# Kernel optimization log

Hardware: AMD Instinct MI355X
Metric: run time of the kernel (lower is better)

The kernel has to match this reference:

```python
import jax, jax.numpy as jnp
import numpy as np

N_NODES = 100000
N_EDGES = 1600000
F_IN = 64
HID = 64
N_ACT = 8


def gcn_conv(x, edge_index, W, b):
    # PyG GCNConv: h = x @ W; add self-loops; norm = deg^{-1/2}[src]*deg^{-1/2}[dst];
    # out[dst] += norm * h[src]; out += b
    n = x.shape[0]
    h = x @ W  # [N, out]
    row = jnp.concatenate([edge_index[0], jnp.arange(n)])  # src (+ self loops)
    col = jnp.concatenate([edge_index[1], jnp.arange(n)])  # dst (+ self loops)
    deg = jax.ops.segment_sum(jnp.ones_like(col, dtype=h.dtype), col, num_segments=n)
    dinv = jnp.where(deg > 0, jax.lax.rsqrt(deg), 0.0)
    norm = dinv[row] * dinv[col]  # [E+N]
    msg = h[row] * norm[:, None]  # gather + scale
    out = jax.ops.segment_sum(msg, col, num_segments=n)  # scatter-add
    return out + b


def setup_inputs() -> dict:
    key = jax.random.key(0)
    ks = jax.random.split(key, 8)
    x = jax.random.normal(ks[0], (N_NODES, F_IN), dtype=jnp.float32)
    edge_index = jax.random.randint(ks[1], (2, N_EDGES), 0, N_NODES, dtype=jnp.int64)
    def glorot(k, fan_in, fan_out):
        s = jnp.sqrt(6.0 / (fan_in + fan_out))
        return jax.random.uniform(k, (fan_in, fan_out), jnp.float32, -s, s)
    W1 = glorot(ks[2], F_IN, HID)
    b1 = jnp.zeros((HID,), jnp.float32)
    W2 = glorot(ks[3], HID, HID)
    b2 = jnp.zeros((HID,), jnp.float32)
    Wfc = glorot(ks[4], HID, N_ACT)
    bfc = jnp.zeros((N_ACT,), jnp.float32)
    return {"x": x, "edge_index": edge_index, "W1": W1, "b1": b1,
            "W2": W2, "b2": b2, "Wfc": Wfc, "bfc": bfc}


def reference(x, edge_index, W1, b1, W2, b2, Wfc, bfc):
    h = jax.nn.relu(gcn_conv(x, edge_index, W1, b1))
    h = jax.nn.relu(gcn_conv(h, edge_index, W2, b2))
    return h @ Wfc + bfc  # Q-values per node: [N, num_actions]
```

## Files before the change

kernel.cpp:

```cpp
#include <hip/hip_runtime.h>
#include <hip/hip_fp16.h>


#define F 64
#define NACT 8
#define BSH 9
#define BNODES 512
#define CAP 10240
#define EPB 2048

__global__ __launch_bounds__(256) void k_init(int* flag, int* cursor) {
  if (threadIdx.x == 0) *flag = 1;
  cursor[threadIdx.x] = 0;
}

__global__ __launch_bounds__(256) void k_detect(const unsigned int* __restrict__ w, int* flag, int E) {
  int i = blockIdx.x * 256 + threadIdx.x;
  if (i < E && w[2 * i + 1] != 0u) *flag = 0;
}

__device__ __forceinline__ int edge_row(const unsigned int* w, int flag, int e, int E) {
  return flag ? (int)w[2 * e] : (int)w[e];
}
__device__ __forceinline__ int edge_col(const unsigned int* w, int flag, int e, int E) {
  return flag ? (int)w[2 * E + 2 * e] : (int)w[E + e];
}

__global__ __launch_bounds__(256) void k_scatterE(const unsigned int* __restrict__ w,
    const int* __restrict__ flag, int* __restrict__ cursor, unsigned int* __restrict__ slab, int E) {
  __shared__ int hist[256];
  __shared__ int base[256];
  const int tid = threadIdx.x;
  const int fl = *flag;
  hist[tid] = 0;
  __syncthreads();
  int pk[8], bb[8], lr[8];
  const int e0 = blockIdx.x * EPB;
#pragma unroll 8
  for (int j = 0; j < 8; ++j) {
    int e = e0 + j * 256 + tid;
    bb[j] = -1;
    if (e < E) {
      int c = edge_col(w, fl, e, E);
      int s = edge_row(w, fl, e, E);
      int b = c >> BSH;
      pk[j] = (unsigned)s | ((unsigned)(c & (BNODES - 1)) << 17);
      bb[j] = b;
      lr[j] = atomicAdd(&hist[b], 1);
    }
  }
  __syncthreads();
  int h = hist[tid];
  if (h > 0) base[tid] = atomicAdd(&cursor[tid], h);
  __syncthreads();
#pragma unroll 8
  for (int j = 0; j < 8; ++j) {
    if (bb[j] >= 0) {
      slab[(size_t)bb[j] * CAP + base[bb[j]] + lr[j]] = (unsigned)pk[j];
    }
  }
}

__global__ __launch_bounds__(64) void k_slabscan(const int* __restrict__ cursor,
    int* __restrict__ bucketBase, int* __restrict__ csr_off, int NB, int n, int E) {
  int t = threadIdx.x;
  int per = (NB + 63) / 64;
  int base = t * per;
  int local = 0;
  for (int i = 0; i < per; ++i) if (base + i < NB) local += cursor[base + i];
  int inc = local;
  for (int off = 1; off < 64; off <<= 1) {
    int vv = __shfl_up(inc, off);
    if (t >= off) inc += vv;
  }
  int run = inc - local;
  for (int i = 0; i < per; ++i) if (base + i < NB) { bucketBase[base + i] = run; run += cursor[base + i]; }
  if (t == 63) { bucketBase[NB] = inc; csr_off[n] = E; }
}

__global__ __launch_bounds__(256) void k_bucketcsr(const unsigned int* __restrict__ slab,
    const int* __restrict__ bucketBase, int* __restrict__ csr_off, float* __restrict__ dinv,
    int* __restrict__ csr_src, int n) {
  __shared__ int cnt[BNODES];
  __shared__ int off[BNODES];
  __shared__ int sA[256], sB[256];
  const int tid = threadIdx.x;
  const int b = blockIdx.x;
  const int csrbeg = bucketBase[b];
  const int cntb = bucketBase[b + 1] - csrbeg;
  const unsigned int* sl = &slab[(size_t)b * CAP];
  cnt[tid] = 0;
  cnt[tid + 256] = 0;
  __syncthreads();
  for (int i = tid; i < cntb; i += 256) {
    atomicAdd(&cnt[sl[i] >> 17], 1);
  }
  __syncthreads();
  int c0 = cnt[2 * tid], c1 = cnt[2 * tid + 1];
  int p = c0 + c1;
  sA[tid] = p;
  __syncthreads();
  int* srcb = sA;
  int* dstb = sB;
  for (int o = 1; o < 256; o <<= 1) {
    int v = srcb[tid];
    if (tid >= o) v += srcb[tid - o];
    __syncthreads();
    dstb[tid] = v;
    __syncthreads();
    int* t2 = srcb; srcb = dstb; dstb = t2;
  }
  int ex2 = srcb[tid] - p;
  off[2 * tid] = ex2;
  off[2 * tid + 1] = ex2 + c0;
  __syncthreads();
  int v0 = (b << BSH) + 2 * tid;
  if (v0 < n) { csr_off[v0] = csrbeg + off[2 * tid]; dinv[v0] = rsqrtf((float)(c0 + 1)); }
  if (v0 + 1 < n) { csr_off[v0 + 1] = csrbeg + off[2 * tid + 1]; dinv[v0 + 1] = rsqrtf((float)(c1 + 1)); }
  __syncthreads();
  for (int i = tid; i < cntb; i += 256) {
    unsigned int pk = sl[i];
    int dl = pk >> 17;
    int pos = atomicAdd(&off[dl], 1);
    csr_src[csrbeg + pos] = (int)(pk & 0x1FFFFu);
  }
}

__device__ __forceinline__ ushort4 packh4(float a, float b, float c, float d) {
  ushort4 r;
  r.x = __half_as_ushort(__float2half_rn(a));
  r.y = __half_as_ushort(__float2half_rn(b));
  r.z = __half_as_ushort(__float2half_rn(c));
  r.w = __half_as_ushort(__float2half_rn(d));
  return r;
}

__device__ __forceinline__ void addrow8(float* a, uint4 g) {
  union { uint4 u; __half2 h[4]; } u;
  u.u = g;
#pragma unroll
  for (int i = 0; i < 4; ++i) {
    float2 f = __half22float2(u.h[i]);
    a[2 * i] += f.x;
    a[2 * i + 1] += f.y;
  }
}

__global__ __launch_bounds__(256) void k_gemm_h(const float* __restrict__ X, const float* __restrict__ W,
    const float* __restrict__ dinv, unsigned short* __restrict__ Gh, int n) {
  __shared__ float xst[F * 68];
  __shared__ float wsh[F * F];
  const int tid = threadIdx.x;
  const int row0 = blockIdx.x * 64;
  for (int i = tid * 4; i < F * F; i += 1024)
    *(float4*)&wsh[i] = *(const float4*)&W[i];
  for (int i = tid * 4; i < 64 * F; i += 1024) {
    int r = i >> 6, k = i & 63;
    float4 v = make_float4(0.f, 0.f, 0.f, 0.f);
    if (row0 + r < n) v = *(const float4*)&X[(size_t)(row0 + r) * F + k];
    xst[(k + 0) * 68 + r] = v.x;
    xst[(k + 1) * 68 + r] = v.y;
    xst[(k + 2) * 68 + r] = v.z;
    xst[(k + 3) * 68 + r] = v.w;
  }
  __syncthreads();
  const int tc = tid & 15;
  const int tr = tid >> 4;
  float a00 = 0.f, a01 = 0.f, a02 = 0.f, a03 = 0.f;
  float a10 = 0.f, a11 = 0.f, a12 = 0.f, a13 = 0.f;
  float a20 = 0.f, a21 = 0.f, a22 = 0.f, a23 = 0.f;
  float a30 = 0.f, a31 = 0.f, a32 = 0.f, a33 = 0.f;
  const float* xp = &xst[tr * 4];
  const float* wp = &wsh[tc * 4];
#pragma unroll 8
  for (int k = 0; k < F; ++k) {
    float4 xv = *(const float4*)&xp[k * 68];
    float4 wv = *(const float4*)&wp[k * F];
    a00 = fmaf(xv.x, wv.x, a00); a01 = fmaf(xv.x, wv.y, a01);
    a02 = fmaf(xv.x, wv.z, a02); a03 = fmaf(xv.x, wv.w, a03);
    a10 = fmaf(xv.y, wv.x, a10); a11 = fmaf(xv.y, wv.y, a11);
    a12 = fmaf(xv.y, wv.z, a12); a13 = fmaf(xv.y, wv.w, a13);
    a20 = fmaf(xv.z, wv.x, a20); a21 = fmaf(xv.z, wv.y, a21);
    a22 = fmaf(xv.z, wv.z, a22); a23 = fmaf(xv.z, wv.w, a23);
    a30 = fmaf(xv.w, wv.x, a30); a31 = fmaf(xv.w, wv.y, a31);
    a32 = fmaf(xv.w, wv.z, a32); a33 = fmaf(xv.w, wv.w, a33);
  }
  const int gc = tc * 4;
  int gr = row0 + tr * 4;
  if (gr + 0 < n) { float d = dinv[gr + 0]; *(ushort4*)&Gh[(size_t)(gr + 0) * F + gc] = packh4(a00 * d, a01 * d, a02 * d, a03 * d); }
  if (gr + 1 < n) { float d = dinv[gr + 1]; *(ushort4*)&Gh[(size_t)(gr + 1) * F + gc] = packh4(a10 * d, a11 * d, a12 * d, a13 * d); }
  if (gr + 2 < n) { float d = dinv[gr + 2]; *(ushort4*)&Gh[(size_t)(gr + 2) * F + gc] = packh4(a20 * d, a21 * d, a22 * d, a23 * d); }
  if (gr + 3 < n) { float d = dinv[gr + 3]; *(ushort4*)&Gh[(size_t)(gr + 3) * F + gc] = packh4(a30 * d, a31 * d, a32 * d, a33 * d); }
}

__global__ __launch_bounds__(256) void k_gather_h(const int* __restrict__ csr_off,
    const int* __restrict__ csr_src, const unsigned short* __restrict__ Gh,
    const float* __restrict__ dinv, const float* __restrict__ b, float* __restrict__ H, int n) {
  int v = blockIdx.x * 32 + (threadIdx.x >> 3);
  if (v >= n) return;
  int l = threadIdx.x & 7;
  const uint4* Gv = (const uint4*)Gh;
  float a[8] = {0.f, 0.f, 0.f, 0.f, 0.f, 0.f, 0.f, 0.f};
  addrow8(a, Gv[(size_t)v * 8 + l]);
  int beg = csr_off[v], end = csr_off[v + 1];
  int j = beg;
  for (; j + 4 <= end; j += 4) {
    int s0 = csr_src[j], s1 = csr_src[j + 1], s2 = csr_src[j + 2], s3 = csr_src[j + 3];
    uint4 g0 = Gv[(size_t)s0 * 8 + l];
    uint4 g1 = Gv[(size_t)s1 * 8 + l];
    uint4 g2 = Gv[(size_t)s2 * 8 + l];
    uint4 g3 = Gv[(size_t)s3 * 8 + l];
    addrow8(a, g0); addrow8(a, g1); addrow8(a, g2); addrow8(a, g3);
  }
  for (; j < end; ++j) addrow8(a, Gv[(size_t)csr_src[j] * 8 + l]);
  float d = dinv[v];
  float4 b0 = *(const float4*)&b[l * 8];
  float4 b1 = *(const float4*)&b[l * 8 + 4];
  float4 o0, o1;
  o0.x = fmaxf(fmaf(a[0], d, b0.x), 0.f);
  o0.y = fmaxf(fmaf(a[1], d, b0.y), 0.f);
  o0.z = fmaxf(fmaf(a[2], d, b0.z), 0.f);
  o0.w = fmaxf(fmaf(a[3], d, b0.w), 0.f);
  o1.x = fmaxf(fmaf(a[4], d, b1.x), 0.f);
  o1.y = fmaxf(fmaf(a[5], d, b1.y), 0.f);
  o1.z = fmaxf(fmaf(a[6], d, b1.z), 0.f);
  o1.w = fmaxf(fmaf(a[7], d, b1.w), 0.f);
  *(float4*)&H[(size_t)v * F + l * 8] = o0;
  *(float4*)&H[(size_t)v * F + l * 8 + 4] = o1;
}

__global__ __launch_bounds__(256) void k_gather_fc(const int* __restrict__ csr_off,
    const int* __restrict__ csr_src, const unsigned short* __restrict__ Gh,
    const float* __restrict__ dinv, const float* __restrict__ bias,
    const float* __restrict__ Wfc, const float* __restrict__ bfc,
    float* __restrict__ OUT, int n) {
  __shared__ float wsh[F * 9];
  __shared__ float bs[NACT];
  const int tid = threadIdx.x;
  for (int i = tid; i < F * NACT; i += 256) wsh[(i >> 3) * 9 + (i & 7)] = Wfc[i];
  if (tid < NACT) bs[tid] = bfc[tid];
  __syncthreads();
  int v = blockIdx.x * 32 + (tid >> 3);
  int l = tid & 7;
  if (v >= n) return;
  const uint4* Gv = (const uint4*)Gh;
  float a[8] = {0.f, 0.f, 0.f, 0.f, 0.f, 0.f, 0.f, 0.f};
  addrow8(a, Gv[(size_t)v * 8 + l]);
  int beg = csr_off[v], end = csr_off[v + 1];
  int j = beg;
  for (; j + 4 <= end; j += 4) {
    int s0 = csr_src[j], s1 = csr_src[j + 1], s2 = csr_src[j + 2], s3 = csr_src[j + 3];
    uint4 g0 = Gv[(size_t)s0 * 8 + l];
    uint4 g1 = Gv[(size_t)s1 * 8 + l];
    uint4 g2 = Gv[(size_t)s2 * 8 + l];
    uint4 g3 = Gv[(size_t)s3 * 8 + l];
    addrow8(a, g0); addrow8(a, g1); addrow8(a, g2); addrow8(a, g3);
  }
  for (; j < end; ++j) addrow8(a, Gv[(size_t)csr_src[j] * 8 + l]);
  float d = dinv[v];
  float q[NACT] = {0.f, 0.f, 0.f, 0.f, 0.f, 0.f, 0.f, 0.f};
#pragma unroll
  for (int jj = 0; jj < 8; ++jj) {
    float h = fmaxf(fmaf(a[jj], d, bias[l * 8 + jj]), 0.f);
    const float* wr = &wsh[(l * 8 + jj) * 9];
#pragma unroll
    for (int aa = 0; aa < NACT; ++aa) q[aa] = fmaf(h, wr[aa], q[aa]);
  }
#pragma unroll
  for (int m = 1; m < 8; m <<= 1) {
#pragma unroll
    for (int aa = 0; aa < NACT; ++aa) q[aa] += __shfl_xor(q[aa], m);
  }
  OUT[(size_t)v * NACT + l] = q[l] + bs[l];
}

extern "C" void kernel_launch(void* const* d_in, const int* in_sizes, int n_in,
                              void* d_out, int out_size, void* d_ws, size_t ws_size,
                              hipStream_t stream) {
  const float* x = (const float*)d_in[0];
  const unsigned int* ew = (const unsigned int*)d_in[1];
  const float* W1 = (const float*)d_in[2];
  const float* b1 = (const float*)d_in[3];
  const float* W2 = (const float*)d_in[4];
  const float* b2 = (const float*)d_in[5];
  const float* Wfc = (const float*)d_in[6];
  const float* bfc = (const float*)d_in[7];
  float* out = (float*)d_out;
  const int n = in_sizes[0] / F;
  const int E = in_sizes[1] / 2;
  const int NB = (n + BNODES - 1) >> BSH;

  char* base = (char*)d_ws;
  size_t off = 0;
  auto alloc = [&](size_t bytes) { void* p = base + off; off += (bytes + 255) & ~(size_t)255; return p; };
  int* flag = (int*)alloc(4);
  int* cursor = (int*)alloc(256 * 4);
  int* bucketBase = (int*)alloc((size_t)(NB + 1) * 4);
  int* csr_off = (int*)alloc((size_t)(n + 1) * 4);
  float* dinv = (float*)alloc((size_t)n * 4);
  unsigned int* slab = (unsigned int*)alloc((size_t)NB * CAP * 4);
  int* csr_src = (int*)alloc((size_t)E * 4);
  unsigned short* Gh = (unsigned short*)alloc((size_t)n * F * 2);
  float* H = (float*)alloc((size_t)n * F * 4);

  const int gbE = (E + 255) / 256;
  const int gbSc = (E + EPB - 1) / EPB;
  const int gbRow = (n + 63) / 64;
  const int gbGa = (n + 31) / 32;

  hipLaunchKernelGGL(k_init, dim3(1), dim3(256), 0, stream, flag, cursor);
  hipLaunchKernelGGL(k_detect, dim3(gbE), dim3(256), 0, stream, ew, flag, E);
  hipLaunchKernelGGL(k_scatterE, dim3(gbSc), dim3(256), 0, stream, ew, flag, cursor, slab, E);
  hipLaunchKernelGGL(k_slabscan, dim3(1), dim3(64), 0, stream, cursor, bucketBase, csr_off, NB, n, E);
  hipLaunchKernelGGL(k_bucketcsr, dim3(NB), dim3(256), 0, stream, slab, bucketBase, csr_off, dinv, csr_src, n);

  hipLaunchKernelGGL(k_gemm_h, dim3(gbRow), dim3(256), 0, stream, x, W1, dinv, Gh, n);
  hipLaunchKernelGGL(k_gather_h, dim3(gbGa), dim3(256), 0, stream, csr_off, csr_src, Gh, dinv, b1, H, n);
  hipLaunchKernelGGL(k_gemm_h, dim3(gbRow), dim3(256), 0, stream, H, W2, dinv, Gh, n);
  hipLaunchKernelGGL(k_gather_fc, dim3(gbGa), dim3(256), 0, stream, csr_off, csr_src, Gh, dinv, b2, Wfc, bfc, out, n);
}
```

Measured before the change: 170.1 us.

## Fuse layer-1 gather with layer-2 GEMM and deepen gather unroll

Merges the first aggregation kernel and the second dense transform into one kernel: each block gathers neighbour rows for 64 nodes, applies bias and ReLU into shared memory, then multiplies by W2 and writes scaled fp16 features directly. This removes the fp32 intermediate H write and read-back plus one launch. It also factors the gather loop into a helper unrolled by 8 for more loads in flight. In exchange it adds 33KB of shared memory per 512-thread block, which may lower occupancy for the latency-bound gather.

```diff
diff --git a/kernel.cpp b/kernel.cpp
--- a/kernel.cpp
+++ b/kernel.cpp
@@ -8,6 +8,7 @@
 #define BNODES 512
 #define CAP 10240
 #define EPB 2048
+#define HS 67
 
 __global__ __launch_bounds__(256) void k_init(int* flag, int* cursor) {
   if (threadIdx.x == 0) *flag = 1;
@@ -144,6 +145,31 @@
     a[2 * i] += f.x;
     a[2 * i + 1] += f.y;
   }
+}
+
+__device__ __forceinline__ void gather8(const uint4* __restrict__ Gv,
+    const int* __restrict__ csr_src, int beg, int end, int l, float* a) {
+  int j = beg;
+  for (; j + 8 <= end; j += 8) {
+    uint4 g0 = Gv[(size_t)csr_src[j + 0] * 8 + l];
+    uint4 g1 = Gv[(size_t)csr_src[j + 1] * 8 + l];
+    uint4 g2 = Gv[(size_t)csr_src[j + 2] * 8 + l];
+    uint4 g3 = Gv[(size_t)csr_src[j + 3] * 8 + l];
+    uint4 g4 = Gv[(size_t)csr_src[j + 4] * 8 + l];
+    uint4 g5 = Gv[(size_t)csr_src[j + 5] * 8 + l];
+    uint4 g6 = Gv[(size_t)csr_src[j + 6] * 8 + l];
+    uint4 g7 = Gv[(size_t)csr_src[j + 7] * 8 + l];
+    addrow8(a, g0); addrow8(a, g1); addrow8(a, g2); addrow8(a, g3);
+    addrow8(a, g4); addrow8(a, g5); addrow8(a, g6); addrow8(a, g7);
+  }
+  for (; j + 4 <= end; j += 4) {
+    uint4 g0 = Gv[(size_t)csr_src[j + 0] * 8 + l];
+    uint4 g1 = Gv[(size_t)csr_src[j + 1] * 8 + l];
+    uint4 g2 = Gv[(size_t)csr_src[j + 2] * 8 + l];
+    uint4 g3 = Gv[(size_t)csr_src[j + 3] * 8 + l];
+    addrow8(a, g0); addrow8(a, g1); addrow8(a, g2); addrow8(a, g3);
+  }
+  for (; j < end; ++j) addrow8(a, Gv[(size_t)csr_src[j] * 8 + l]);
 }
 
 __global__ __launch_bounds__(256) void k_gemm_h(const float* __restrict__ X, const float* __restrict__ W,
@@ -193,40 +219,58 @@
   if (gr + 3 < n) { float d = dinv[gr + 3]; *(ushort4*)&Gh[(size_t)(gr + 3) * F + gc] = packh4(a30 * d, a31 * d, a32 * d, a33 * d); }
 }
 
-__global__ __launch_bounds__(256) void k_gather_h(const int* __restrict__ csr_off,
-    const int* __restrict__ csr_src, const unsigned short* __restrict__ Gh,
-    const float* __restrict__ dinv, const float* __restrict__ b, float* __restrict__ H, int n) {
-  int v = blockIdx.x * 32 + (threadIdx.x >> 3);
-  if (v >= n) return;
-  int l = threadIdx.x & 7;
-  const uint4* Gv = (const uint4*)Gh;
+__global__ __launch_bounds__(512) void k_gather_gemm(const int* __restrict__ csr_off,
+    const int* __restrict__ csr_src, const unsigned short* __restrict__ Gh1,
+    const float* __restrict__ dinv, const float* __restrict__ bias,
+    const float* __restrict__ W2, unsigned short* __restrict__ Gh2, int n) {
+  __shared__ float hst[F * HS];
+  __shared__ float wsh[F * F];
+  const int tid = threadIdx.x;
+  const int row0 = blockIdx.x * 64;
+  {
+    int i = tid * 8;
+    *(float4*)&wsh[i] = *(const float4*)&W2[i];
+    *(float4*)&wsh[i + 4] = *(const float4*)&W2[i + 4];
+  }
+  const int ln = tid >> 3;
+  const int l = tid & 7;
+  const int v = row0 + ln;
   float a[8] = {0.f, 0.f, 0.f, 0.f, 0.f, 0.f, 0.f, 0.f};
-  addrow8(a, Gv[(size_t)v * 8 + l]);
-  int beg = csr_off[v], end = csr_off[v + 1];
-  int j = beg;
-  for (; j + 4 <= end; j += 4) {
-    int s0 = csr_src[j], s1 = csr_src[j + 1], s2 = csr_src[j + 2], s3 = csr_src[j + 3];
-    uint4 g0 = Gv[(size_t)s0 * 8 + l];
-    uint4 g1 = Gv[(size_t)s1 * 8 + l];
-    uint4 g2 = Gv[(size_t)s2 * 8 + l];
-    uint4 g3 = Gv[(size_t)s3 * 8 + l];
-    addrow8(a, g0); addrow8(a, g1); addrow8(a, g2); addrow8(a, g3);
-  }
-  for (; j < end; ++j) addrow8(a, Gv[(size_t)csr_src[j] * 8 + l]);
-  float d = dinv[v];
-  float4 b0 = *(const float4*)&b[l * 8];
-  float4 b1 = *(const float4*)&b[l * 8 + 4];
-  float4 o0, o1;
-  o0.x = fmaxf(fmaf(a[0], d, b0.x), 0.f);
-  o0.y = fmaxf(fmaf(a[1], d, b0.y), 0.f);
-  o0.z = fmaxf(fmaf(a[2], d, b0.z), 0.f);
-  o0.w = fmaxf(fmaf(a[3], d, b0.w), 0.f);
-  o1.x = fmaxf(fmaf(a[4], d, b1.x), 0.f);
-  o1.y = fmaxf(fmaf(a[5], d, b1.y), 0.f);
-  o1.z = fmaxf(fmaf(a[6], d, b1.z), 0.f);
-  o1.w = fmaxf(fmaf(a[7], d, b1.w), 0.f);
-  *(float4*)&H[(size_t)v * F + l * 8] = o0;
-  *(float4*)&H[(size_t)v * F + l * 8 + 4] = o1;
+  if (v < n) {
+    const uint4* Gv = (const uint4*)Gh1;
+    addrow8(a, Gv[(size_t)v * 8 + l]);
+    gather8(Gv, csr_src, csr_off[v], csr_off[v + 1], l, a);
+    float d = dinv[v];
+#pragma unroll
+    for (int jj = 0; jj < 8; ++jj) {
+      float h = fmaxf(fmaf(a[jj], d, bias[l * 8 + jj]), 0.f);
+      hst[(l * 8 + jj) * HS + ln] = h;
+    }
+  } else {
+#pragma unroll
+    for (int jj = 0; jj < 8; ++jj) hst[(l * 8 + jj) * HS + ln] = 0.f;
+  }
+  __syncthreads();
+  const int tc = tid & 15;
+  const int tr = tid >> 4;
+  const int r0 = 2 * tr;
+  float a00 = 0.f, a01 = 0.f, a02 = 0.f, a03 = 0.f;
+  float a10 = 0.f, a11 = 0.f, a12 = 0.f, a13 = 0.f;
+  const float* wp = &wsh[tc * 4];
+#pragma unroll 8
+  for (int k = 0; k < F; ++k) {
+    float h0 = hst[k * HS + r0];
+    float h1 = hst[k * HS + r0 + 1];
+    float4 wv = *(const float4*)&wp[k * F];
+    a00 = fmaf(h0, wv.x, a00); a01 = fmaf(h0, wv.y, a01);
+    a02 = fmaf(h0, wv.z, a02); a03 = fmaf(h0, wv.w, a03);
+    a10 = fmaf(h1, wv.x, a10); a11 = fmaf(h1, wv.y, a11);
+    a12 = fmaf(h1, wv.z, a12); a13 = fmaf(h1, wv.w, a13);
+  }
+  const int gc = tc * 4;
+  int gr = row0 + r0;
+  if (gr < n) { float d = dinv[gr]; *(ushort4*)&Gh2[(size_t)gr * F + gc] = packh4(a00 * d, a01 * d, a02 * d, a03 * d); }
+  if (gr + 1 < n) { float d = dinv[gr + 1]; *(ushort4*)&Gh2[(size_t)(gr + 1) * F + gc] = packh4(a10 * d, a11 * d, a12 * d, a13 * d); }
 }
 
 __global__ __launch_bounds__(256) void k_gather_fc(const int* __restrict__ csr_off,
@@ -246,17 +290,7 @@
   const uint4* Gv = (const uint4*)Gh;
   float a[8] = {0.f, 0.f, 0.f, 0.f, 0.f, 0.f, 0.f, 0.f};
   addrow8(a, Gv[(size_t)v * 8 + l]);
-  int beg = csr_off[v], end = csr_off[v + 1];
-  int j = beg;
-  for (; j + 4 <= end; j += 4) {
-    int s0 = csr_src[j], s1 = csr_src[j + 1], s2 = csr_src[j + 2], s3 = csr_src[j + 3];
-    uint4 g0 = Gv[(size_t)s0 * 8 + l];
-    uint4 g1 = Gv[(size_t)s1 * 8 + l];
-    uint4 g2 = Gv[(size_t)s2 * 8 + l];
-    uint4 g3 = Gv[(size_t)s3 * 8 + l];
-    addrow8(a, g0); addrow8(a, g1); addrow8(a, g2); addrow8(a, g3);
-  }
-  for (; j < end; ++j) addrow8(a, Gv[(size_t)csr_src[j] * 8 + l]);
+  gather8(Gv, csr_src, csr_off[v], csr_off[v + 1], l, a);
   float d = dinv[v];
   float q[NACT] = {0.f, 0.f, 0.f, 0.f, 0.f, 0.f, 0.f, 0.f};
 #pragma unroll
@@ -300,8 +334,8 @@
   float* dinv = (float*)alloc((size_t)n * 4);
   unsigned int* slab = (unsigned int*)alloc((size_t)NB * CAP * 4);
   int* csr_src = (int*)alloc((size_t)E * 4);
-  unsigned short* Gh = (unsigned short*)alloc((size_t)n * F * 2);
-  float* H = (float*)alloc((size_t)n * F * 4);
+  unsigned short* Gh1 = (unsigned short*)alloc((size_t)n * F * 2);
+  unsigned short* Gh2 = (unsigned short*)alloc((size_t)n * F * 2);
 
   const int gbE = (E + 255) / 256;
   const int gbSc = (E + EPB - 1) / EPB;
@@ -314,8 +348,7 @@
   hipLaunchKernelGGL(k_slabscan, dim3(1), dim3(64), 0, stream, cursor, bucketBase, csr_off, NB, n, E);
   hipLaunchKernelGGL(k_bucketcsr, dim3(NB), dim3(256), 0, stream, slab, bucketBase, csr_off, dinv, csr_src, n);
 
-  hipLaunchKernelGGL(k_gemm_h, dim3(gbRow), dim3(256), 0, stream, x, W1, dinv, Gh, n);
-  hipLaunchKernelGGL(k_gather_h, dim3(gbGa), dim3(256), 0, stream, csr_off, csr_src, Gh, dinv, b1, H, n);
-  hipLaunchKernelGGL(k_gemm_h, dim3(gbRow), dim3(256), 0, stream, H, W2, dinv, Gh, n);
-  hipLaunchKernelGGL(k_gather_fc, dim3(gbGa), dim3(256), 0, stream, csr_off, csr_src, Gh, dinv, b2, Wfc, bfc, out, n);
-}
+  hipLaunchKernelGGL(k_gemm_h, dim3(gbRow), dim3(256), 0, stream, x, W1, dinv, Gh1, n);
+  hipLaunchKernelGGL(k_gather_gemm, dim3(gbRow), dim3(512), 0, stream, csr_off, csr_src, Gh1, dinv, b1, W2, Gh2, n);
+  hipLaunchKernelGGL(k_gather_fc, dim3(gbGa), dim3(256), 0, stream, csr_off, csr_src, Gh2, dinv, b2, Wfc, bfc, out, n);
+}
```

Result: faster. 163.8 us (-3.7%).
